# Optimization experiments

Measured on AMD Instinct MI355X. Metric: run time of the kernel, lower is better.

The kernel has to match this reference:

```python
import jax, jax.numpy as jnp
import numpy as np

B, S, HID = 2, 2048, 1024
NH = 16
HD = HID // NH  # 64
ROPE_BASE = 10000.0
NEG_INF = -1e9


def _rope_emb(seq_len):
    # emb = cat(sin, cos) over head_dim, shape [1, S, 1, HD]
    inv_freq = 1.0 / (ROPE_BASE ** (jnp.arange(0, HD, 2, dtype=jnp.float32) / HD))
    pos = jnp.arange(seq_len, dtype=jnp.float32)
    sincos = pos[:, None] * inv_freq[None, :]            # [S, HD/2]
    emb = jnp.concatenate([jnp.sin(sincos), jnp.cos(sincos)], axis=-1)  # [S, HD]
    return emb[None, :, None, :]


def _apply_rope(x, emb):
    # Faithful to the (quirky) torch code: cos = emb[..., 1::2], sin = emb[..., ::2]
    cos = emb[..., 1::2]
    sin = emb[..., ::2]
    xe = x[..., ::2]
    xo = x[..., 1::2]
    return jnp.concatenate([xe * cos - xo * sin, xe * sin + xo * cos], axis=-1)


def setup_inputs() -> dict:
    key = jax.random.key(0)
    ks = jax.random.split(key, 5)
    hidden_states = jax.random.normal(ks[0], (B, S, HID), dtype=jnp.float32)
    # causal additive mask, broadcast over batch/heads
    causal = jnp.tril(jnp.ones((S, S), dtype=bool))
    attention_mask = jnp.where(causal, 0.0, NEG_INF).astype(jnp.float32)[None, None]
    scale = 1.0 / np.sqrt(HID)
    w_q = jax.random.normal(ks[1], (HID, HID), dtype=jnp.float32) * scale
    w_k = jax.random.normal(ks[2], (HID, HID), dtype=jnp.float32) * scale
    w_v = jax.random.normal(ks[3], (HID, HID), dtype=jnp.float32) * scale
    w_o = jax.random.normal(ks[4], (HID, HID), dtype=jnp.float32) * scale
    return {"hidden_states": hidden_states, "attention_mask": attention_mask,
            "w_q": w_q, "w_k": w_k, "w_v": w_v, "w_o": w_o}


def reference(hidden_states, attention_mask, w_q, w_k, w_v, w_o):
    b, s, _ = hidden_states.shape
    # torch Linear: x @ W.T (W is [out, in])
    q = (hidden_states @ w_q.T).reshape(b, s, NH, HD)
    k = (hidden_states @ w_k.T).reshape(b, s, NH, HD)
    v = (hidden_states @ w_v.T).reshape(b, s, NH, HD)
    emb = _rope_emb(s)
    q = _apply_rope(q, emb)
    k = _apply_rope(k, emb)
    # [b, h, s, d]
    q = q.transpose(0, 2, 1, 3)
    k = k.transpose(0, 2, 1, 3)
    v = v.transpose(0, 2, 1, 3)
    scores = jnp.einsum('bhqd,bhkd->bhqk', q, k) / np.sqrt(HD)
    scores = scores + attention_mask
    attn = jax.nn.softmax(scores, axis=-1)
    out = jnp.einsum('bhqk,bhkd->bhqd', attn, v)
    out = out.transpose(0, 2, 1, 3).reshape(b, s, HID)
    return out @ w_o.T
```

## Files before the change

### kernel.cpp

```cpp
#include <hip/hip_runtime.h>
#include <hip/hip_bf16.h>
#include <math.h>

typedef unsigned short u16;
typedef unsigned int   u32;
typedef unsigned long long u64;
typedef __attribute__((ext_vector_type(8))) short bf16x8;
typedef __attribute__((ext_vector_type(4))) short bf16x4;
typedef __attribute__((ext_vector_type(4))) float f32x4;

#define B_   2
#define S_   2048
#define HID_ 1024
#define NH_  16
#define HD_  64
#define MR_  (B_*S_)

#define QSCALE 0.1803368801111137f

__device__ __forceinline__ u16 f2bf(float f) {
  union { float f; u32 u; } x; x.f = f;
  u32 r = x.u + 0x7fffu + ((x.u >> 16) & 1u);
  return (u16)(r >> 16);
}
__device__ __forceinline__ void gload16(const void* g, void* l) {
  __builtin_amdgcn_global_load_lds(
      (const __attribute__((address_space(1))) u32*)g,
      (__attribute__((address_space(3))) u32*)l, 16, 0, 0);
}

__global__ void k_cvt_all(const float* __restrict__ hs, const float* __restrict__ wq,
                          const float* __restrict__ wk, const float* __restrict__ wv,
                          const float* __restrict__ wo, ushort4* __restrict__ dst) {
  int i = blockIdx.x * blockDim.x + threadIdx.x;
  const float4* src;
  int idx;
  if (i < 1048576) {
    src = (const float4*)hs; idx = i;
  } else {
    int j = i - 1048576;
    int w = j >> 18; idx = j & 262143;
    src = (const float4*)(w == 0 ? wq : w == 1 ? wk : w == 2 ? wv : wo);
  }
  float4 v = src[idx];
  ushort4 o;
  o.x = f2bf(v.x); o.y = f2bf(v.y); o.z = f2bf(v.z); o.w = f2bf(v.w);
  dst[i] = o;
}

__global__ void k_rope_table(float2* __restrict__ tab) {
  int t = blockIdx.x * blockDim.x + threadIdx.x;
  int p = t >> 5, j = t & 31;
  double fp = (double)p;
  double c, s;
  if (j < 16) {
    s = sin(fp * pow(10000.0, -(2.0 * j) / 32.0));
    c = sin(fp * pow(10000.0, -(2.0 * j + 1.0) / 32.0));
  } else {
    s = cos(fp * pow(10000.0, -(2.0 * j - 32.0) / 32.0));
    c = cos(fp * pow(10000.0, -(2.0 * j - 31.0) / 32.0));
  }
  tab[p * 32 + j] = make_float2((float)c, (float)s);
}

template <int MODE, int BM>
__global__ __launch_bounds__(256) void k_gemm_bt(
    const u16* __restrict__ A,
    const u16* __restrict__ W0, const u16* __restrict__ W1, const u16* __restrict__ W2,
    u16* __restrict__ O0, u16* __restrict__ O1, u16* __restrict__ O2,
    float* __restrict__ OF, const float2* __restrict__ tab, int K) {
  constexpr int MI = BM / 32;
  constexpr int WR = BM / 2;
  __shared__ __align__(16) u16 Al[BM * 64];
  __shared__ __align__(16) u16 Bl[128 * 64];

  int tid = threadIdx.x;
  int lane = tid & 63, wave = tid >> 6;
  int m0 = blockIdx.y * BM;
  int nt0 = blockIdx.x * 128;
  int wi = nt0 >> 10;
  const u16* W = (wi == 0) ? W0 : (wi == 1 ? W1 : W2);
  int n0 = nt0 & 1023;
  int wm = wave >> 1, wn = wave & 1;
  int lg = lane >> 4, lr = lane & 15;

  f32x4 acc[MI][4];
  const f32x4 vz = {0.f, 0.f, 0.f, 0.f};
#pragma unroll
  for (int i = 0; i < MI; ++i)
#pragma unroll
    for (int j = 0; j < 4; ++j) acc[i][j] = vz;

  int chunk = wave * 64 + lane;

  for (int k0 = 0; k0 < K; k0 += 64) {
#pragma unroll
    for (int it = 0; it < BM / 32; ++it) {
      int c = it * 256 + chunk;
      int row = c >> 3;
      int cw = (c & 7) ^ (row & 7);
      gload16(&A[(size_t)(m0 + row) * K + k0 + cw * 8], &Al[(it * 256 + wave * 64) * 8]);
    }
#pragma unroll
    for (int it = 0; it < 4; ++it) {
      int c = it * 256 + chunk;
      int row = c >> 3;
      int cw = (c & 7) ^ (row & 7);
      gload16(&W[(size_t)(n0 + row) * K + k0 + cw * 8], &Bl[(it * 256 + wave * 64) * 8]);
    }
    __syncthreads();
#pragma unroll
    for (int kk = 0; kk < 2; ++kk) {
      bf16x8 af[MI], bfr[4];
#pragma unroll
      for (int mi = 0; mi < MI; ++mi) {
        int row = wm * WR + mi * 16 + lr;
        int ci = (kk * 4 + lg) ^ (row & 7);
        af[mi] = *(const bf16x8*)&Al[row * 64 + ci * 8];
      }
#pragma unroll
      for (int ni = 0; ni < 4; ++ni) {
        int row = wn * 64 + ni * 16 + lr;
        int ci = (kk * 4 + lg) ^ (row & 7);
        bfr[ni] = *(const bf16x8*)&Bl[row * 64 + ci * 8];
      }
#pragma unroll
      for (int mi = 0; mi < MI; ++mi)
#pragma unroll
        for (int ni = 0; ni < 4; ++ni)
          acc[mi][ni] = __builtin_amdgcn_mfma_f32_16x16x32_bf16(af[mi], bfr[ni], acc[mi][ni], 0, 0, 0);
    }
    __syncthreads();
  }

  if (MODE == 1) {
#pragma unroll
    for (int mi = 0; mi < MI; ++mi)
#pragma unroll
      for (int ni = 0; ni < 4; ++ni)
#pragma unroll
        for (int r = 0; r < 4; ++r) {
          int grow = m0 + wm * WR + mi * 16 + lg * 4 + r;
          int gcol = n0 + wn * 64 + ni * 16 + lr;
          OF[(size_t)grow * 1024 + gcol] = acc[mi][ni][r];
        }
    return;
  }

  if (wi == 2) {
#pragma unroll
    for (int mi = 0; mi < MI; ++mi) {
      int grow0 = m0 + wm * WR + mi * 16 + lg * 4;
      int bb = grow0 >> 11;
      int s = grow0 & 2047;
#pragma unroll
      for (int ni = 0; ni < 4; ++ni) {
        int gcol = n0 + wn * 64 + ni * 16 + lr;
        int h = gcol >> 6, dd = gcol & 63;
        u64 pk = (u64)f2bf(acc[mi][ni][0]) |
                 ((u64)f2bf(acc[mi][ni][1]) << 16) |
                 ((u64)f2bf(acc[mi][ni][2]) << 32) |
                 ((u64)f2bf(acc[mi][ni][3]) << 48);
        *(u64*)&O2[((size_t)(bb * NH_ + h) * HD_ + dd) * S_ + s] = pk;
      }
    }
  } else {
    u16* OB = wi ? O1 : O0;
    float sc = wi ? 1.0f : QSCALE;
#pragma unroll
    for (int mi = 0; mi < MI; ++mi) {
#pragma unroll
      for (int ni = 0; ni < 4; ++ni) {
        int gcol = n0 + wn * 64 + ni * 16 + lr;
        int h = gcol >> 6;
        int j = (gcol & 63) >> 1;
        bool even = !(gcol & 1);
        int ocol = h * 64 + (even ? j : 32 + j);
#pragma unroll
        for (int r = 0; r < 4; ++r) {
          float val = acc[mi][ni][r];
          float pv = __shfl_xor(val, 1);
          int grow = m0 + wm * WR + mi * 16 + lg * 4 + r;
          int s = grow & 2047;
          float2 cs = tab[s * 32 + j];
          float xe = even ? val : pv;
          float xo = even ? pv : val;
          float res = even ? (xe * cs.x - xo * cs.y) : (xe * cs.y + xo * cs.x);
          OB[(size_t)grow * 1024 + ocol] = f2bf(res * sc);
        }
      }
    }
  }
}

__global__ __launch_bounds__(256, 4) void k_attn(
    const u16* __restrict__ Q, const u16* __restrict__ Kr, const u16* __restrict__ VT,
    u16* __restrict__ O) {
  __shared__ __align__(16) u16 Kl[2][64 * 64];
  __shared__ __align__(16) u16 Vl[2][64 * 64];

  int tid = threadIdx.x, lane = tid & 63, wave = tid >> 6;
  int id = blockIdx.x;
  int qt = 31 - (id >> 5);
  int bh = id & 31;
  int b = bh >> 4, h = bh & 15;
  int lg = lane >> 4, lr = lane & 15;
  int bS = b * S_;
  int nkt = qt + 1;
  int q0 = qt * 64 + wave * 16;

  const u16* vtb = &VT[(size_t)bh * HD_ * S_];
  int l8 = lane >> 3, l7 = lane & 7;
  int sl = l7 ^ l8;

  auto STAGE = [&](int kt_, int bs_) {
#pragma unroll
    for (int it = 0; it < 2; ++it) {
      int rb = wave * 16 + it * 8;
      int r = rb + l8;
      gload16(&Kr[(size_t)(bS + kt_ * 64 + r) * HID_ + h * HD_ + sl * 8],
              &Kl[bs_][rb * 64]);
      gload16(&vtb[(size_t)r * S_ + kt_ * 64 + sl * 8],
              &Vl[bs_][rb * 64]);
    }
  };

  STAGE(0, 0);

  bf16x8 qf[2];
#pragma unroll
  for (int kk = 0; kk < 2; ++kk)
    qf[kk] = *(const bf16x8*)
        &Q[(size_t)(bS + q0 + lr) * HID_ + h * HD_ + kk * 32 + lg * 8];

  f32x4 acc[4];
  const f32x4 vz = {0.f, 0.f, 0.f, 0.f};
#pragma unroll
  for (int df = 0; df < 4; ++df) acc[df] = vz;
  float m_ = -1e30f;
  float l_ = 0.f;

  for (int kt = 0; kt < nkt; ++kt) {
    int cur = kt & 1;
    if (kt + 1 < nkt) {
      STAGE(kt + 1, cur ^ 1);
      asm volatile("s_waitcnt vmcnt(4)" ::: "memory");
    } else {
      asm volatile("s_waitcnt vmcnt(0)" ::: "memory");
    }
    __builtin_amdgcn_s_barrier();
    __builtin_amdgcn_sched_barrier(0);

    bf16x8 kfr[4][2];
#pragma unroll
    for (int kf = 0; kf < 4; ++kf) {
      int row = kf * 16 + lr;
#pragma unroll
      for (int kk = 0; kk < 2; ++kk) {
        int ci = (kk * 4 + lg) ^ (row & 7);
        kfr[kf][kk] = *(const bf16x8*)&Kl[cur][row * 64 + ci * 8];
      }
    }

    f32x4 st[4];
#pragma unroll
    for (int kf = 0; kf < 4; ++kf) st[kf] = vz;
    __builtin_amdgcn_s_setprio(1);
#pragma unroll
    for (int kk = 0; kk < 2; ++kk)
#pragma unroll
      for (int kf = 0; kf < 4; ++kf)
        st[kf] = __builtin_amdgcn_mfma_f32_16x16x32_bf16(
            kfr[kf][kk], qf[kk], st[kf], 0, 0, 0);
    __builtin_amdgcn_s_setprio(0);

    if (kt == qt) {
      int qg = q0 + lr;
#pragma unroll
      for (int kf = 0; kf < 4; ++kf)
#pragma unroll
        for (int r = 0; r < 4; ++r) {
          int kg = kt * 64 + kf * 16 + lg * 4 + r;
          if (kg > qg) st[kf][r] = -1e30f;
        }
    }

    float tmx = -1e30f;
#pragma unroll
    for (int kf = 0; kf < 4; ++kf)
#pragma unroll
      for (int r = 0; r < 4; ++r) tmx = fmaxf(tmx, st[kf][r]);
    tmx = fmaxf(tmx, __shfl_xor(tmx, 16));
    tmx = fmaxf(tmx, __shfl_xor(tmx, 32));

    if (!__all(tmx <= m_ + 8.f)) {
      float mn = fmaxf(m_, tmx);
      float rsc = __builtin_amdgcn_exp2f(m_ - mn);
      l_ *= rsc;
#pragma unroll
      for (int df = 0; df < 4; ++df) acc[df] *= rsc;
      m_ = mn;
    }
    float mb = m_;
    float ts = 0.f;
    bf16x4 pb[4];
#pragma unroll
    for (int kf = 0; kf < 4; ++kf) {
#pragma unroll
      for (int r = 0; r < 4; ++r) {
        float e = __builtin_amdgcn_exp2f(st[kf][r] - mb);
        st[kf][r] = e;
        ts += e;
      }
      u32 w0, w1;
      asm("v_cvt_pk_bf16_f32 %0, %1, %2" : "=v"(w0) : "v"(st[kf][0]), "v"(st[kf][1]));
      asm("v_cvt_pk_bf16_f32 %0, %1, %2" : "=v"(w1) : "v"(st[kf][2]), "v"(st[kf][3]));
      union { u32 u[2]; bf16x4 v; } pk;
      pk.u[0] = w0; pk.u[1] = w1;
      pb[kf] = pk.v;
    }
    ts += __shfl_xor(ts, 16);
    ts += __shfl_xor(ts, 32);
    l_ += ts;

    __builtin_amdgcn_s_setprio(1);
#pragma unroll
    for (int df = 0; df < 4; ++df) {
      int row = df * 16 + lr;
#pragma unroll
      for (int kf = 0; kf < 4; ++kf) {
        int slot = (kf * 2 + (lg >> 1)) ^ (row & 7);
        bf16x4 vfr = *(const bf16x4*)&Vl[cur][row * 64 + slot * 8 + (lg & 1) * 4];
        acc[df] = __builtin_amdgcn_mfma_f32_16x16x16bf16_1k(
            vfr, pb[kf], acc[df], 0, 0, 0);
      }
    }
    __builtin_amdgcn_s_setprio(0);

    __builtin_amdgcn_sched_barrier(0);
    __builtin_amdgcn_s_barrier();
  }

  float inv = 1.0f / l_;
  int grow = bS + q0 + lr;
#pragma unroll
  for (int df = 0; df < 4; ++df) {
    u64 pk = (u64)f2bf(acc[df][0] * inv) |
             ((u64)f2bf(acc[df][1] * inv) << 16) |
             ((u64)f2bf(acc[df][2] * inv) << 32) |
             ((u64)f2bf(acc[df][3] * inv) << 48);
    *(u64*)&O[(size_t)grow * HID_ + h * HD_ + df * 16 + lg * 4] = pk;
  }
}

extern "C" void kernel_launch(void* const* d_in, const int* in_sizes, int n_in,
                              void* d_out, int out_size, void* d_ws, size_t ws_size,
                              hipStream_t stream) {
  const float* hs = (const float*)d_in[0];
  const float* wq = (const float*)d_in[2];
  const float* wk = (const float*)d_in[3];
  const float* wv = (const float*)d_in[4];
  const float* wo = (const float*)d_in[5];
  float* out = (float*)d_out;

  char* ws = (char*)d_ws;
  const size_t P = (size_t)MR_ * HID_ * 2;
  u16* Xb  = (u16*)(ws);
  u16* Wqb = (u16*)(ws + P);
  u16* Wkb = (u16*)(ws + P + (size_t)HID_ * HID_ * 2);
  u16* Wvb = (u16*)(ws + P + (size_t)HID_ * HID_ * 4);
  u16* Wob = (u16*)(ws + P + (size_t)HID_ * HID_ * 6);
  u16* q_r = (u16*)(ws + 2 * P);
  u16* k_r = (u16*)(ws + 3 * P);
  u16* vt  = (u16*)(ws + 4 * P);
  float2* tab = (float2*)(ws + 5 * P);
  u16* attn_o = Xb;

  k_cvt_all<<<8192, 256, 0, stream>>>(hs, wq, wk, wv, wo, (ushort4*)ws);
  k_rope_table<<<256, 256, 0, stream>>>(tab);

  k_gemm_bt<0, 128><<<dim3(24, 32), 256, 0, stream>>>(
      Xb, Wqb, Wkb, Wvb, q_r, k_r, vt, nullptr, tab, HID_);

  k_attn<<<1024, 256, 0, stream>>>(q_r, k_r, vt, attn_o);

  k_gemm_bt<1, 64><<<dim3(8, 64), 256, 0, stream>>>(
      attn_o, Wob, Wob, Wob, nullptr, nullptr, nullptr, out, nullptr, HID_);
}
```

Before: 128.9 us.

## Stage QKV GEMM epilogue through LDS for coalesced 16-byte stores

The Q/K/V projection epilogue now writes bf16 results into a swizzled per-wave LDS buffer (reusing the GEMM tile memory) and then emits 16-byte coalesced global stores, replacing scattered 2-byte and 8-byte stores. For Q/K, the MFMA operands are swapped so each lane holds adjacent columns, which lets RoPE pairs be handled in-register without shuffles and with vectorized sin/cos table loads. Conversion uses the hardware packed bf16 instruction. This adds an extra LDS round trip and barrier, and it relies on BM being 128 so each wave's 64x64 tile fits its LDS slice.

```diff
diff --git a/kernel.cpp b/kernel.cpp
--- a/kernel.cpp
+++ b/kernel.cpp
@@ -71,8 +71,9 @@
     float* __restrict__ OF, const float2* __restrict__ tab, int K) {
   constexpr int MI = BM / 32;
   constexpr int WR = BM / 2;
-  __shared__ __align__(16) u16 Al[BM * 64];
-  __shared__ __align__(16) u16 Bl[128 * 64];
+  __shared__ __align__(16) u16 SM[BM * 64 + 128 * 64];
+  u16* Al = SM;
+  u16* Bl = SM + BM * 64;
 
   int tid = threadIdx.x;
   int lane = tid & 63, wave = tid >> 6;
@@ -92,6 +93,7 @@
     for (int j = 0; j < 4; ++j) acc[i][j] = vz;
 
   int chunk = wave * 64 + lane;
+  bool swapped = (MODE == 0) && (wi < 2);
 
   for (int k0 = 0; k0 < K; k0 += 64) {
 #pragma unroll
@@ -124,11 +126,19 @@
         int ci = (kk * 4 + lg) ^ (row & 7);
         bfr[ni] = *(const bf16x8*)&Bl[row * 64 + ci * 8];
       }
-#pragma unroll
-      for (int mi = 0; mi < MI; ++mi)
-#pragma unroll
-        for (int ni = 0; ni < 4; ++ni)
-          acc[mi][ni] = __builtin_amdgcn_mfma_f32_16x16x32_bf16(af[mi], bfr[ni], acc[mi][ni], 0, 0, 0);
+      if (swapped) {
+#pragma unroll
+        for (int mi = 0; mi < MI; ++mi)
+#pragma unroll
+          for (int ni = 0; ni < 4; ++ni)
+            acc[mi][ni] = __builtin_amdgcn_mfma_f32_16x16x32_bf16(bfr[ni], af[mi], acc[mi][ni], 0, 0, 0);
+      } else {
+#pragma unroll
+        for (int mi = 0; mi < MI; ++mi)
+#pragma unroll
+          for (int ni = 0; ni < 4; ++ni)
+            acc[mi][ni] = __builtin_amdgcn_mfma_f32_16x16x32_bf16(af[mi], bfr[ni], acc[mi][ni], 0, 0, 0);
+      }
     }
     __syncthreads();
   }
@@ -147,48 +157,66 @@
     return;
   }
 
+  u16* eb = SM + wave * 4096;
+  int c8 = lane & 7;
+
   if (wi == 2) {
 #pragma unroll
     for (int mi = 0; mi < MI; ++mi) {
-      int grow0 = m0 + wm * WR + mi * 16 + lg * 4;
-      int bb = grow0 >> 11;
-      int s = grow0 & 2047;
 #pragma unroll
       for (int ni = 0; ni < 4; ++ni) {
-        int gcol = n0 + wn * 64 + ni * 16 + lr;
-        int h = gcol >> 6, dd = gcol & 63;
-        u64 pk = (u64)f2bf(acc[mi][ni][0]) |
-                 ((u64)f2bf(acc[mi][ni][1]) << 16) |
-                 ((u64)f2bf(acc[mi][ni][2]) << 32) |
-                 ((u64)f2bf(acc[mi][ni][3]) << 48);
-        *(u64*)&O2[((size_t)(bb * NH_ + h) * HD_ + dd) * S_ + s] = pk;
-      }
+        int dl = ni * 16 + lr;
+        int bir = (2 * (mi * 16 + lg * 4)) ^ ((dl & 7) << 4);
+        u32 lo, hi;
+        asm("v_cvt_pk_bf16_f32 %0, %1, %2" : "=v"(lo) : "v"(acc[mi][ni][0]), "v"(acc[mi][ni][1]));
+        asm("v_cvt_pk_bf16_f32 %0, %1, %2" : "=v"(hi) : "v"(acc[mi][ni][2]), "v"(acc[mi][ni][3]));
+        u64 pk = (u64)lo | ((u64)hi << 32);
+        *(u64*)((char*)eb + dl * 128 + bir) = pk;
+      }
+    }
+    __syncthreads();
+    int bb = m0 >> 11;
+    int s0 = (m0 & 2047) + wm * 64;
+    int h = (n0 + wn * 64) >> 6;
+#pragma unroll
+    for (int i = 0; i < 8; ++i) {
+      int dr = (lane >> 3) + i * 8;
+      f32x4 v = *(f32x4*)((char*)eb + dr * 128 + ((c8 * 16) ^ ((dr & 7) << 4)));
+      *(f32x4*)&O2[((size_t)((bb * NH_ + h) * HD_) + dr) * S_ + s0 + c8 * 8] = v;
     }
   } else {
+    float sc = wi ? 1.0f : QSCALE;
+#pragma unroll
+    for (int mi = 0; mi < MI; ++mi) {
+      int srow = mi * 16 + lr;
+      int s = (m0 + wm * WR + srow) & 2047;
+      const float* tb = (const float*)&tab[s * 32];
+      char* rowp = (char*)eb + srow * 128;
+      int X = (lr & 7) << 4;
+#pragma unroll
+      for (int ni = 0; ni < 4; ++ni) {
+        int jA = ni * 8 + lg * 2;
+        float4 cs2 = *(const float4*)(tb + jA * 2);
+        f32x4 a = acc[mi][ni];
+        float e0 = (a[0] * cs2.x - a[1] * cs2.y) * sc;
+        float o0 = (a[0] * cs2.y + a[1] * cs2.x) * sc;
+        float e1 = (a[2] * cs2.z - a[3] * cs2.w) * sc;
+        float o1 = (a[2] * cs2.w + a[3] * cs2.z) * sc;
+        u32 lo, hi;
+        asm("v_cvt_pk_bf16_f32 %0, %1, %2" : "=v"(lo) : "v"(e0), "v"(e1));
+        asm("v_cvt_pk_bf16_f32 %0, %1, %2" : "=v"(hi) : "v"(o0), "v"(o1));
+        *(u32*)(rowp + ((2 * jA) ^ X)) = lo;
+        *(u32*)(rowp + ((64 + 2 * jA) ^ X)) = hi;
+      }
+    }
+    __syncthreads();
     u16* OB = wi ? O1 : O0;
-    float sc = wi ? 1.0f : QSCALE;
-#pragma unroll
-    for (int mi = 0; mi < MI; ++mi) {
-#pragma unroll
-      for (int ni = 0; ni < 4; ++ni) {
-        int gcol = n0 + wn * 64 + ni * 16 + lr;
-        int h = gcol >> 6;
-        int j = (gcol & 63) >> 1;
-        bool even = !(gcol & 1);
-        int ocol = h * 64 + (even ? j : 32 + j);
-#pragma unroll
-        for (int r = 0; r < 4; ++r) {
-          float val = acc[mi][ni][r];
-          float pv = __shfl_xor(val, 1);
-          int grow = m0 + wm * WR + mi * 16 + lg * 4 + r;
-          int s = grow & 2047;
-          float2 cs = tab[s * 32 + j];
-          float xe = even ? val : pv;
-          float xo = even ? pv : val;
-          float res = even ? (xe * cs.x - xo * cs.y) : (xe * cs.y + xo * cs.x);
-          OB[(size_t)grow * 1024 + ocol] = f2bf(res * sc);
-        }
-      }
+    int colb = n0 + wn * 64 + c8 * 8;
+#pragma unroll
+    for (int i = 0; i < 8; ++i) {
+      int sr = (lane >> 3) + i * 8;
+      f32x4 v = *(f32x4*)((char*)eb + sr * 128 + ((c8 * 16) ^ ((sr & 7) << 4)));
+      *(f32x4*)&OB[(size_t)(m0 + wm * 64 + sr) * 1024 + colb] = v;
     }
   }
 }
```

Measured after the change: 151.3 us. 1.17x slower.

## Double-buffer GEMM LDS tiles with async prefetch and manual waitcnt

Applied to the files above, without the earlier changes.

Converts the projection GEMM's k-loop to double-buffered LDS, issuing global-to-LDS loads for the next k-tile before computing the current one. Explicit vmcnt waits and raw barriers replace __syncthreads, so memory latency can overlap MFMA work. It also raises wave priority around the MFMA block. The cost is twice the LDS per block, which may lower occupancy. The hard-coded vmcnt values depend on the per-stage load counts (8 for MODE 0, 6 otherwise) and would break if BM changed.

```diff
diff --git a/kernel.cpp b/kernel.cpp
--- a/kernel.cpp
+++ b/kernel.cpp
@@ -71,8 +71,8 @@
     float* __restrict__ OF, const float2* __restrict__ tab, int K) {
   constexpr int MI = BM / 32;
   constexpr int WR = BM / 2;
-  __shared__ __align__(16) u16 Al[BM * 64];
-  __shared__ __align__(16) u16 Bl[128 * 64];
+  __shared__ __align__(16) u16 Al[2][BM * 64];
+  __shared__ __align__(16) u16 Bl[2][128 * 64];
 
   int tid = threadIdx.x;
   int lane = tid & 63, wave = tid >> 6;
@@ -93,22 +93,39 @@
 
   int chunk = wave * 64 + lane;
 
-  for (int k0 = 0; k0 < K; k0 += 64) {
+  auto STAGE = [&](int t_, int bs_) {
+    int k0 = t_ * 64;
 #pragma unroll
     for (int it = 0; it < BM / 32; ++it) {
       int c = it * 256 + chunk;
       int row = c >> 3;
       int cw = (c & 7) ^ (row & 7);
-      gload16(&A[(size_t)(m0 + row) * K + k0 + cw * 8], &Al[(it * 256 + wave * 64) * 8]);
+      gload16(&A[(size_t)(m0 + row) * K + k0 + cw * 8], &Al[bs_][(it * 256 + wave * 64) * 8]);
     }
 #pragma unroll
     for (int it = 0; it < 4; ++it) {
       int c = it * 256 + chunk;
       int row = c >> 3;
       int cw = (c & 7) ^ (row & 7);
-      gload16(&W[(size_t)(n0 + row) * K + k0 + cw * 8], &Bl[(it * 256 + wave * 64) * 8]);
-    }
-    __syncthreads();
+      gload16(&W[(size_t)(n0 + row) * K + k0 + cw * 8], &Bl[bs_][(it * 256 + wave * 64) * 8]);
+    }
+  };
+
+  int nkt = K >> 6;
+  STAGE(0, 0);
+
+  for (int t = 0; t < nkt; ++t) {
+    int cur = t & 1;
+    if (t + 1 < nkt) {
+      STAGE(t + 1, cur ^ 1);
+      if (MODE == 0) asm volatile("s_waitcnt vmcnt(8)" ::: "memory");
+      else           asm volatile("s_waitcnt vmcnt(6)" ::: "memory");
+    } else {
+      asm volatile("s_waitcnt vmcnt(0)" ::: "memory");
+    }
+    __builtin_amdgcn_s_barrier();
+    __builtin_amdgcn_sched_barrier(0);
+
 #pragma unroll
     for (int kk = 0; kk < 2; ++kk) {
       bf16x8 af[MI], bfr[4];
@@ -116,21 +133,24 @@
       for (int mi = 0; mi < MI; ++mi) {
         int row = wm * WR + mi * 16 + lr;
         int ci = (kk * 4 + lg) ^ (row & 7);
-        af[mi] = *(const bf16x8*)&Al[row * 64 + ci * 8];
+        af[mi] = *(const bf16x8*)&Al[cur][row * 64 + ci * 8];
       }
 #pragma unroll
       for (int ni = 0; ni < 4; ++ni) {
         int row = wn * 64 + ni * 16 + lr;
         int ci = (kk * 4 + lg) ^ (row & 7);
-        bfr[ni] = *(const bf16x8*)&Bl[row * 64 + ci * 8];
-      }
+        bfr[ni] = *(const bf16x8*)&Bl[cur][row * 64 + ci * 8];
+      }
+      __builtin_amdgcn_s_setprio(1);
 #pragma unroll
       for (int mi = 0; mi < MI; ++mi)
 #pragma unroll
         for (int ni = 0; ni < 4; ++ni)
           acc[mi][ni] = __builtin_amdgcn_mfma_f32_16x16x32_bf16(af[mi], bfr[ni], acc[mi][ni], 0, 0, 0);
-    }
-    __syncthreads();
+      __builtin_amdgcn_s_setprio(0);
+    }
+    __builtin_amdgcn_sched_barrier(0);
+    __builtin_amdgcn_s_barrier();
   }
 
   if (MODE == 1) {
```

After: 123.9 us. 3.9% less time.
